# Optimization experiments

Hardware: AMD Instinct MI355X
Metric: run time of the kernel (lower is better)

## Reference

```python
import jax, jax.numpy as jnp
import numpy as np

D_MODEL = 1024
NUM_HEADS = 16
D_K = D_MODEL // NUM_HEADS
B, T = 2, 2048


def setup_inputs() -> dict:
    key = jax.random.key(0)
    ks = jax.random.split(key, 9)
    s = 1.0 / np.sqrt(D_MODEL)
    inp = {"x": jax.random.normal(ks[0], (B, T, D_MODEL), dtype=jnp.float32)}
    for i, name in enumerate(["q", "k", "v", "out"]):
        inp[f"W_{name}"] = jax.random.uniform(ks[1 + 2 * i], (D_MODEL, D_MODEL), jnp.float32, -s, s)
        inp[f"b_{name}"] = jax.random.uniform(ks[2 + 2 * i], (D_MODEL,), jnp.float32, -s, s)
    return inp


def reference(x, W_q, b_q, W_k, b_k, W_v, b_v, W_out, b_out):
    b, t, _ = x.shape
    # torch Linear: y = x @ W.T + b
    def proj(inp, W, bias):
        y = inp @ W.T + bias
        return y.reshape(b, -1, NUM_HEADS, D_K).transpose(0, 2, 1, 3)  # [B,H,T,d_k]

    Q = proj(x, W_q, b_q)
    K = proj(x, W_k, b_k)
    V = proj(x, W_v, b_v)
    scores = jnp.einsum("bhqd,bhkd->bhqk", Q, K) / jnp.sqrt(jnp.float32(D_K))
    attn = jax.nn.softmax(scores, axis=-1)
    ctx = jnp.einsum("bhqk,bhkd->bhqd", attn, V)
    ctx = ctx.transpose(0, 2, 1, 3).reshape(b, t, D_MODEL)
    return ctx @ W_out.T + b_out
```

## Files before the change

### kernel.cpp

```cpp
#include <hip/hip_runtime.h>
#include <hip/hip_bf16.h>

typedef __attribute__((ext_vector_type(8))) short short8;
typedef __attribute__((ext_vector_type(4))) short short4v;
typedef __attribute__((ext_vector_type(4))) float floatx4;

__device__ __forceinline__ unsigned short f2b(float f) {
  unsigned int v;
  __builtin_memcpy(&v, &f, 4);
  unsigned int r = (v + 0x7FFFu + ((v >> 16) & 1u)) >> 16;
  return (unsigned short)r;
}

__device__ __forceinline__ unsigned int f2b_pk(float a, float b) {
#if __has_builtin(__builtin_amdgcn_cvt_pk_bf16_f32)
  typedef __attribute__((ext_vector_type(2))) __bf16 bf16x2;
  bf16x2 r = __builtin_amdgcn_cvt_pk_bf16_f32(a, b);
  unsigned int u;
  __builtin_memcpy(&u, &r, 4);
  return u;
#else
  return ((unsigned int)f2b(b) << 16) | (unsigned int)f2b(a);
#endif
}

__device__ __forceinline__ float fast_exp2(float x) {
#if __has_builtin(__builtin_amdgcn_exp2f)
  return __builtin_amdgcn_exp2f(x);
#else
  return __builtin_exp2f(x);
#endif
}

__device__ __forceinline__ void async_copy16(const void* g, void* l) {
  __builtin_amdgcn_global_load_lds(
      (const __attribute__((address_space(1))) unsigned int*)g,
      (__attribute__((address_space(3))) unsigned int*)l, 16, 0, 0);
}

#define QSCALE 0.18033688011112042f

__global__ __launch_bounds__(256) void cvt_all_kernel(
    const float* __restrict__ x,
    const float* __restrict__ w0, const float* __restrict__ w1,
    const float* __restrict__ w2, const float* __restrict__ w3,
    unsigned short* __restrict__ xb,
    unsigned short* __restrict__ d0, unsigned short* __restrict__ d1,
    unsigned short* __restrict__ d2, unsigned short* __restrict__ d3)
{
  int gid = blockIdx.x * 256 + threadIdx.x;
  const float* src;
  unsigned short* dst;
  size_t off;
  if (gid < (1 << 20)) {
    src = x; dst = xb; off = gid;
  } else {
    int g = gid - (1 << 20);
    int w = g >> 18;
    off = g & 0x3FFFF;
    src = (w == 0) ? w0 : (w == 1) ? w1 : (w == 2) ? w2 : w3;
    dst = (w == 0) ? d0 : (w == 1) ? d1 : (w == 2) ? d2 : d3;
  }
  floatx4 v = *(const floatx4*)(src + off * 4);
  unsigned int lo = f2b_pk(v[0], v[1]), hi = f2b_pk(v[2], v[3]);
  unsigned long long r = ((unsigned long long)hi << 32) | lo;
  *(unsigned long long*)(dst + off * 4) = r;
}

__global__ __launch_bounds__(256) void gemm_qkv_kernel(
    const unsigned short* __restrict__ A,
    const unsigned short* __restrict__ W0, const unsigned short* __restrict__ W1,
    const unsigned short* __restrict__ W2,
    const float* __restrict__ bias0, const float* __restrict__ bias1,
    const float* __restrict__ bias2,
    unsigned short* __restrict__ Qo, unsigned short* __restrict__ Ko,
    unsigned short* __restrict__ VTo)
{
  const int z = blockIdx.z;
  const unsigned short* W  = (z == 0) ? W0 : (z == 1) ? W1 : W2;
  const float* bias        = (z == 0) ? bias0 : (z == 1) ? bias1 : bias2;

  __shared__ alignas(16) unsigned short sA[128 * 32];
  __shared__ alignas(16) unsigned short sB[128 * 32];

  const int tid  = threadIdx.x;
  const int lane = tid & 63;
  const int wave = tid >> 6;
  const int col  = lane & 15;
  const int quad = lane >> 4;
  const int wm   = (wave >> 1) * 64;
  const int wn   = (wave & 1) * 64;
  const int m0   = blockIdx.y * 128;
  const int n0   = blockIdx.x * 128;

  floatx4 acc[4][4];
#pragma unroll
  for (int i = 0; i < 4; ++i)
#pragma unroll
    for (int j = 0; j < 4; ++j) acc[i][j] = (floatx4){0.f, 0.f, 0.f, 0.f};

  for (int k0 = 0; k0 < 1024; k0 += 32) {
    __syncthreads();
#pragma unroll
    for (int i = 0; i < 2; ++i) {
      int c   = i * 256 + tid;
      int row = c >> 2;
      int ko  = (c & 3) * 8;
      async_copy16(A + (size_t)(m0 + row) * 1024 + k0 + ko, sA + c * 8);
      async_copy16(W + (size_t)(n0 + row) * 1024 + k0 + ko, sB + c * 8);
    }
    __syncthreads();
    short8 af[4], bf[4];
#pragma unroll
    for (int mi = 0; mi < 4; ++mi)
      af[mi] = *(const short8*)(sA + (wm + mi * 16 + col) * 32 + quad * 8);
#pragma unroll
    for (int ni = 0; ni < 4; ++ni)
      bf[ni] = *(const short8*)(sB + (wn + ni * 16 + col) * 32 + quad * 8);
#pragma unroll
    for (int mi = 0; mi < 4; ++mi)
#pragma unroll
      for (int ni = 0; ni < 4; ++ni)
        acc[mi][ni] = __builtin_amdgcn_mfma_f32_16x16x32_bf16(af[mi], bf[ni], acc[mi][ni], 0, 0, 0);
  }

#pragma unroll
  for (int ni = 0; ni < 4; ++ni) {
    int n = n0 + wn + ni * 16 + col;
    float bv = bias[n];
#pragma unroll
    for (int mi = 0; mi < 4; ++mi) {
      int mbase = m0 + wm + mi * 16 + quad * 4;
#pragma unroll
      for (int r = 0; r < 4; ++r) {
        int m = mbase + r;
        float val = acc[mi][ni][r] + bv;
        if (z == 0) {
          Qo[(size_t)m * 1024 + n] = f2b(val * QSCALE);
        } else if (z == 1) {
          Ko[(size_t)m * 1024 + n] = f2b(val);
        } else {
          int d = n & 63, h = n >> 6;
          int bb = m >> 11, t = m & 2047;
          VTo[(((size_t)bb * 16 + h) * 64 + d) * 2048 + t] = f2b(val);
        }
      }
    }
  }
}

__global__ __launch_bounds__(256) void gemm_out_kernel(
    const unsigned short* __restrict__ A, const unsigned short* __restrict__ W,
    const float* __restrict__ bias, float* __restrict__ DF)
{
  __shared__ alignas(16) unsigned short sA[128 * 32];
  __shared__ alignas(16) unsigned short sB[64 * 32];

  const int tid  = threadIdx.x;
  const int lane = tid & 63;
  const int wave = tid >> 6;
  const int col  = lane & 15;
  const int quad = lane >> 4;
  const int wm   = (wave >> 1) * 64;
  const int wn   = (wave & 1) * 32;
  const int m0   = blockIdx.y * 128;
  const int n0   = blockIdx.x * 64;

  floatx4 acc[4][2];
#pragma unroll
  for (int i = 0; i < 4; ++i)
#pragma unroll
    for (int j = 0; j < 2; ++j) acc[i][j] = (floatx4){0.f, 0.f, 0.f, 0.f};

  for (int k0 = 0; k0 < 1024; k0 += 32) {
    __syncthreads();
#pragma unroll
    for (int i = 0; i < 2; ++i) {
      int c   = i * 256 + tid;
      int row = c >> 2;
      int ko  = (c & 3) * 8;
      async_copy16(A + (size_t)(m0 + row) * 1024 + k0 + ko, sA + c * 8);
    }
    {
      int row = tid >> 2;
      int ko  = (tid & 3) * 8;
      async_copy16(W + (size_t)(n0 + row) * 1024 + k0 + ko, sB + tid * 8);
    }
    __syncthreads();
    short8 af[4], bf[2];
#pragma unroll
    for (int mi = 0; mi < 4; ++mi)
      af[mi] = *(const short8*)(sA + (wm + mi * 16 + col) * 32 + quad * 8);
#pragma unroll
    for (int ni = 0; ni < 2; ++ni)
      bf[ni] = *(const short8*)(sB + (wn + ni * 16 + col) * 32 + quad * 8);
#pragma unroll
    for (int mi = 0; mi < 4; ++mi)
#pragma unroll
      for (int ni = 0; ni < 2; ++ni)
        acc[mi][ni] = __builtin_amdgcn_mfma_f32_16x16x32_bf16(af[mi], bf[ni], acc[mi][ni], 0, 0, 0);
  }

#pragma unroll
  for (int ni = 0; ni < 2; ++ni) {
    int n = n0 + wn + ni * 16 + col;
    float bv = bias[n];
#pragma unroll
    for (int mi = 0; mi < 4; ++mi) {
      int mbase = m0 + wm + mi * 16 + quad * 4;
#pragma unroll
      for (int r = 0; r < 4; ++r)
        DF[(size_t)(mbase + r) * 1024 + n] = acc[mi][ni][r] + bv;
    }
  }
}

__global__ __launch_bounds__(256) void attention_kernel(
    const unsigned short* __restrict__ Q, const unsigned short* __restrict__ K,
    const unsigned short* __restrict__ VT, unsigned short* __restrict__ CTX)
{
  __shared__ alignas(16) unsigned short sKb[16384];
  __shared__ alignas(16) unsigned short sVb[8192];
  __shared__ alignas(16) unsigned short sPb[9216];
  __shared__ float sL[4][64];

  const int bh = blockIdx.x;
  const int b = bh >> 4, h = bh & 15;
  const int q0 = blockIdx.y * 64;
  const int tid  = threadIdx.x;
  const int lane = tid & 63;
  const int wave = tid >> 6;
  const int col  = lane & 15;
  const int quad = lane >> 4;
  const int l4   = lane >> 2;
  const int lo4  = (lane & 3) * 8;

  const unsigned short* Kg = K + (size_t)(b * 2048) * 1024 + h * 64;
  const unsigned short* Vg = VT + (size_t)bh * 64 * 2048;

#pragma unroll
  for (int s = 0; s < 2; ++s)
    async_copy16(Q + (size_t)(b * 2048 + q0 + wave * 16 + l4) * 1024 + h * 64 + s * 32 + lo4,
                 sPb + s * 2048 + wave * 512 + lane * 8);
  {
    unsigned short* kd = sKb + wave * 2048;
#pragma unroll
    for (int s = 0; s < 2; ++s)
#pragma unroll
      for (int j = 0; j < 2; ++j)
        async_copy16(Kg + (size_t)(wave * 32 + j * 16 + l4) * 1024 + s * 32 + lo4,
                     kd + s * 1024 + j * 512 + lane * 8);
    unsigned short* vd = sVb + wave * 2048;
#pragma unroll
    for (int i = 0; i < 4; ++i)
      async_copy16(Vg + (size_t)(i * 16 + l4) * 2048 + wave * 32 + lo4,
                   vd + i * 512 + lane * 8);
  }
  __builtin_amdgcn_s_waitcnt(0xF70);
  __syncthreads();

  short8 qf[4][2];
#pragma unroll
  for (int qc = 0; qc < 4; ++qc)
#pragma unroll
    for (int s = 0; s < 2; ++s)
      qf[qc][s] = *(const short8*)(sPb + s * 2048 + (qc * 16 + col) * 32 + quad * 8);
  __syncthreads();

  floatx4 Oacc[4][4];
#pragma unroll
  for (int mq = 0; mq < 4; ++mq)
#pragma unroll
    for (int nd = 0; nd < 4; ++nd) Oacc[mq][nd] = (floatx4){0.f, 0.f, 0.f, 0.f};
  float lacc[4] = {0.f, 0.f, 0.f, 0.f};
  unsigned short* myP = sPb + wave * 2304;
  unsigned short* vw  = sVb + wave * 2048;

  for (int t = 0; t < 16; ++t) {
    const int buf = t & 1;
    unsigned short* kw = sKb + buf * 8192 + wave * 2048;
    const int ktn = (t + 1) * 128;

    if (t < 15) {
      unsigned short* kd = sKb + (buf ^ 1) * 8192 + wave * 2048;
#pragma unroll
      for (int s = 0; s < 2; ++s)
#pragma unroll
        for (int j = 0; j < 2; ++j)
          async_copy16(Kg + (size_t)(ktn + wave * 32 + j * 16 + l4) * 1024 + s * 32 + lo4,
                       kd + s * 1024 + j * 512 + lane * 8);
      __builtin_amdgcn_s_waitcnt(0xF78);
    } else {
      __builtin_amdgcn_s_waitcnt(0xF74);
    }

    floatx4 ST[2][4];
#pragma unroll
    for (int kr = 0; kr < 2; ++kr)
#pragma unroll
      for (int qc = 0; qc < 4; ++qc) ST[kr][qc] = (floatx4){0.f, 0.f, 0.f, 0.f};
#pragma unroll
    for (int s = 0; s < 2; ++s) {
      short8 k0 = *(const short8*)(kw + s * 1024 + col * 32 + quad * 8);
      short8 k1 = *(const short8*)(kw + s * 1024 + (16 + col) * 32 + quad * 8);
#pragma unroll
      for (int qc = 0; qc < 4; ++qc) {
        ST[0][qc] = __builtin_amdgcn_mfma_f32_16x16x32_bf16(k0, qf[qc][s], ST[0][qc], 0, 0, 0);
        ST[1][qc] = __builtin_amdgcn_mfma_f32_16x16x32_bf16(k1, qf[qc][s], ST[1][qc], 0, 0, 0);
      }
    }

#pragma unroll
    for (int kr = 0; kr < 2; ++kr)
#pragma unroll
      for (int qc = 0; qc < 4; ++qc) {
        float p0 = fast_exp2(ST[kr][qc][0]);
        float p1 = fast_exp2(ST[kr][qc][1]);
        float p2 = fast_exp2(ST[kr][qc][2]);
        float p3 = fast_exp2(ST[kr][qc][3]);
        lacc[qc] += (p0 + p1) + (p2 + p3);
        unsigned long long pw =
            ((unsigned long long)f2b_pk(p2, p3) << 32) | f2b_pk(p0, p1);
        *(unsigned long long*)(myP + (qc * 16 + col) * 36 + kr * 16 + quad * 4) = pw;
      }

    short8 pf[4];
#pragma unroll
    for (int mq = 0; mq < 4; ++mq) {
      const unsigned short* pp = myP + (mq * 16 + col) * 36 + quad * 8;
      short4v plo = *(const short4v*)pp;
      short4v phi = *(const short4v*)(pp + 4);
      pf[mq] = (short8){plo[0], plo[1], plo[2], plo[3], phi[0], phi[1], phi[2], phi[3]};
    }

    if (t < 15) __builtin_amdgcn_s_waitcnt(0xF74);
    else        __builtin_amdgcn_s_waitcnt(0xF70);

    short8 vf[4];
#pragma unroll
    for (int nd = 0; nd < 4; ++nd)
      vf[nd] = *(const short8*)(vw + (nd * 16 + col) * 32 + quad * 8);
    __builtin_amdgcn_s_waitcnt(0xC07F);

    if (t < 15) {
#pragma unroll
      for (int i = 0; i < 4; ++i)
        async_copy16(Vg + (size_t)(i * 16 + l4) * 2048 + ktn + wave * 32 + lo4,
                     vw + i * 512 + lane * 8);
    }

#pragma unroll
    for (int nd = 0; nd < 4; ++nd)
#pragma unroll
      for (int mq = 0; mq < 4; ++mq)
        Oacc[mq][nd] = __builtin_amdgcn_mfma_f32_16x16x32_bf16(pf[mq], vf[nd], Oacc[mq][nd], 0, 0, 0);
  }

#pragma unroll
  for (int qc = 0; qc < 4; ++qc) {
    lacc[qc] += __shfl_xor(lacc[qc], 16, 64);
    lacc[qc] += __shfl_xor(lacc[qc], 32, 64);
  }
  if (quad == 0) {
#pragma unroll
    for (int qc = 0; qc < 4; ++qc) sL[wave][qc * 16 + col] = lacc[qc];
  }

  float* sO = (float*)sKb;
#pragma unroll 1
  for (int ww = 0; ww < 4; ++ww) {
    __syncthreads();
    if (wave == ww) {
#pragma unroll
      for (int mq = 0; mq < 4; ++mq)
#pragma unroll
        for (int nd = 0; nd < 4; ++nd)
#pragma unroll
          for (int r = 0; r < 4; ++r) {
            int idx = (mq * 16 + quad * 4 + r) * 64 + nd * 16 + col;
            if (ww == 0) sO[idx] = Oacc[mq][nd][r];
            else         sO[idx] += Oacc[mq][nd][r];
          }
    }
  }
  __syncthreads();

  {
    int q = tid >> 2, c = tid & 3;
    float l = sL[0][q] + sL[1][q] + sL[2][q] + sL[3][q];
    float inv = 1.f / l;
    const float* row = sO + q * 64 + c * 16;
    unsigned short* dst = CTX + (size_t)(b * 2048 + q0 + q) * 1024 + h * 64 + c * 16;
#pragma unroll
    for (int hf = 0; hf < 2; ++hf) {
      alignas(16) unsigned short ob[8];
#pragma unroll
      for (int j = 0; j < 8; ++j) ob[j] = f2b(row[hf * 8 + j] * inv);
      *(short8*)(dst + hf * 8) = *(const short8*)ob;
    }
  }
}

extern "C" void kernel_launch(void* const* d_in, const int* in_sizes, int n_in,
                              void* d_out, int out_size, void* d_ws, size_t ws_size,
                              hipStream_t stream) {
  const float* x   = (const float*)d_in[0];
  const float* W_q = (const float*)d_in[1];
  const float* b_q = (const float*)d_in[2];
  const float* W_k = (const float*)d_in[3];
  const float* b_k = (const float*)d_in[4];
  const float* W_v = (const float*)d_in[5];
  const float* b_v = (const float*)d_in[6];
  const float* W_o = (const float*)d_in[7];
  const float* b_o = (const float*)d_in[8];
  float* out = (float*)d_out;

  const size_t NX = (size_t)4096 * 1024;
  const size_t NW = (size_t)1024 * 1024;

  unsigned short* p   = (unsigned short*)d_ws;
  unsigned short* xb  = p;  p += NX;
  unsigned short* Wqb = p;  p += NW;
  unsigned short* Wkb = p;  p += NW;
  unsigned short* Wvb = p;  p += NW;
  unsigned short* Wob = p;  p += NW;
  unsigned short* Q   = p;  p += NX;
  unsigned short* Kb  = p;  p += NX;
  unsigned short* VT  = p;  p += NX;
  unsigned short* CTX = p;  p += NX;

  dim3 blk(256);
  cvt_all_kernel<<<dim3(8192), blk, 0, stream>>>(
      x, W_q, W_k, W_v, W_o, xb, Wqb, Wkb, Wvb, Wob);
  gemm_qkv_kernel<<<dim3(8, 32, 3), blk, 0, stream>>>(
      xb, Wqb, Wkb, Wvb, b_q, b_k, b_v, Q, Kb, VT);
  attention_kernel<<<dim3(32, 32), blk, 0, stream>>>(Q, Kb, VT, CTX);
  gemm_out_kernel<<<dim3(16, 32), blk, 0, stream>>>(CTX, Wob, b_o, out);
}
```

Measured before the change: 229.2 us.

## Load K/V fragments directly to registers and keep P in registers via transposed MFMA

The attention kernel drops the shared-memory staging of K and V tiles and the async copies. Each wave now loads its K and V MFMA fragments straight from global memory into double-buffered registers. The second GEMM is computed transposed (V^T times P), so the bf16 probabilities feed the MFMA from registers instead of round-tripping through LDS. Launch bounds request two blocks per SM. In exchange, global loads are less coalesced, register pressure is higher, and latency hiding now depends on the register prefetch.

```diff
diff --git a/kernel.cpp b/kernel.cpp
--- a/kernel.cpp
+++ b/kernel.cpp
@@ -215,13 +215,11 @@
   }
 }
 
-__global__ __launch_bounds__(256) void attention_kernel(
+__global__ __launch_bounds__(256, 2) void attention_kernel(
     const unsigned short* __restrict__ Q, const unsigned short* __restrict__ K,
     const unsigned short* __restrict__ VT, unsigned short* __restrict__ CTX)
 {
-  __shared__ alignas(16) unsigned short sKb[16384];
-  __shared__ alignas(16) unsigned short sVb[8192];
-  __shared__ alignas(16) unsigned short sPb[9216];
+  __shared__ float sO[64 * 64];
   __shared__ float sL[4][64];
 
   const int bh = blockIdx.x;
@@ -232,129 +230,97 @@
   const int wave = tid >> 6;
   const int col  = lane & 15;
   const int quad = lane >> 4;
-  const int l4   = lane >> 2;
-  const int lo4  = (lane & 3) * 8;
-
-  const unsigned short* Kg = K + (size_t)(b * 2048) * 1024 + h * 64;
-  const unsigned short* Vg = VT + (size_t)bh * 64 * 2048;
-
-#pragma unroll
-  for (int s = 0; s < 2; ++s)
-    async_copy16(Q + (size_t)(b * 2048 + q0 + wave * 16 + l4) * 1024 + h * 64 + s * 32 + lo4,
-                 sPb + s * 2048 + wave * 512 + lane * 8);
-  {
-    unsigned short* kd = sKb + wave * 2048;
+
+  const unsigned short* Kg  = K + ((size_t)b * 2048) * 1024 + h * 64;
+  const unsigned short* VTg = VT + (size_t)bh * 64 * 2048;
+
+  short8 qf[4][2];
+#pragma unroll
+  for (int qc = 0; qc < 4; ++qc)
 #pragma unroll
     for (int s = 0; s < 2; ++s)
-#pragma unroll
-      for (int j = 0; j < 2; ++j)
-        async_copy16(Kg + (size_t)(wave * 32 + j * 16 + l4) * 1024 + s * 32 + lo4,
-                     kd + s * 1024 + j * 512 + lane * 8);
-    unsigned short* vd = sVb + wave * 2048;
-#pragma unroll
-    for (int i = 0; i < 4; ++i)
-      async_copy16(Vg + (size_t)(i * 16 + l4) * 2048 + wave * 32 + lo4,
-                   vd + i * 512 + lane * 8);
-  }
-  __builtin_amdgcn_s_waitcnt(0xF70);
-  __syncthreads();
-
-  short8 qf[4][2];
-#pragma unroll
-  for (int qc = 0; qc < 4; ++qc)
-#pragma unroll
-    for (int s = 0; s < 2; ++s)
-      qf[qc][s] = *(const short8*)(sPb + s * 2048 + (qc * 16 + col) * 32 + quad * 8);
-  __syncthreads();
+      qf[qc][s] = *(const short8*)(Q + (size_t)(b * 2048 + q0 + qc * 16 + col) * 1024
+                                    + h * 64 + s * 32 + quad * 8);
 
   floatx4 Oacc[4][4];
 #pragma unroll
-  for (int mq = 0; mq < 4; ++mq)
-#pragma unroll
-    for (int nd = 0; nd < 4; ++nd) Oacc[mq][nd] = (floatx4){0.f, 0.f, 0.f, 0.f};
+  for (int nd = 0; nd < 4; ++nd)
+#pragma unroll
+    for (int qc = 0; qc < 4; ++qc) Oacc[nd][qc] = (floatx4){0.f, 0.f, 0.f, 0.f};
   float lacc[4] = {0.f, 0.f, 0.f, 0.f};
-  unsigned short* myP = sPb + wave * 2304;
-  unsigned short* vw  = sVb + wave * 2048;
-
+
+  short8  kfb[2][2][2];
+  short4v vfb[2][4][2];
+
+  const int ksl = wave * 32;
+
+#define LOAD_K(buf, kt)                                                        \
+  {                                                                            \
+    _Pragma("unroll") for (int kr = 0; kr < 2; ++kr)                           \
+      _Pragma("unroll") for (int s = 0; s < 2; ++s)                            \
+        kfb[buf][kr][s] = *(const short8*)(                                    \
+            Kg + (size_t)((kt) + ksl + kr * 16 + col) * 1024 + s * 32 + quad * 8); \
+  }
+#define LOAD_V(buf, kt)                                                        \
+  {                                                                            \
+    _Pragma("unroll") for (int nd = 0; nd < 4; ++nd)                           \
+      _Pragma("unroll") for (int hf = 0; hf < 2; ++hf)                         \
+        vfb[buf][nd][hf] = *(const short4v*)(                                  \
+            VTg + (size_t)(nd * 16 + col) * 2048 + (kt) + ksl + hf * 16 + quad * 4); \
+  }
+
+  LOAD_K(0, 0)
+  LOAD_V(0, 0)
+
+#pragma unroll 2
   for (int t = 0; t < 16; ++t) {
-    const int buf = t & 1;
-    unsigned short* kw = sKb + buf * 8192 + wave * 2048;
-    const int ktn = (t + 1) * 128;
-
+    const int cur = t & 1, nxt = cur ^ 1;
     if (t < 15) {
-      unsigned short* kd = sKb + (buf ^ 1) * 8192 + wave * 2048;
-#pragma unroll
-      for (int s = 0; s < 2; ++s)
-#pragma unroll
-        for (int j = 0; j < 2; ++j)
-          async_copy16(Kg + (size_t)(ktn + wave * 32 + j * 16 + l4) * 1024 + s * 32 + lo4,
-                       kd + s * 1024 + j * 512 + lane * 8);
-      __builtin_amdgcn_s_waitcnt(0xF78);
-    } else {
-      __builtin_amdgcn_s_waitcnt(0xF74);
+      LOAD_K(nxt, (t + 1) * 128)
+      LOAD_V(nxt, (t + 1) * 128)
     }
 
     floatx4 ST[2][4];
 #pragma unroll
     for (int kr = 0; kr < 2; ++kr)
 #pragma unroll
-      for (int qc = 0; qc < 4; ++qc) ST[kr][qc] = (floatx4){0.f, 0.f, 0.f, 0.f};
-#pragma unroll
-    for (int s = 0; s < 2; ++s) {
-      short8 k0 = *(const short8*)(kw + s * 1024 + col * 32 + quad * 8);
-      short8 k1 = *(const short8*)(kw + s * 1024 + (16 + col) * 32 + quad * 8);
-#pragma unroll
       for (int qc = 0; qc < 4; ++qc) {
-        ST[0][qc] = __builtin_amdgcn_mfma_f32_16x16x32_bf16(k0, qf[qc][s], ST[0][qc], 0, 0, 0);
-        ST[1][qc] = __builtin_amdgcn_mfma_f32_16x16x32_bf16(k1, qf[qc][s], ST[1][qc], 0, 0, 0);
+        ST[kr][qc] = (floatx4){0.f, 0.f, 0.f, 0.f};
+        ST[kr][qc] = __builtin_amdgcn_mfma_f32_16x16x32_bf16(
+            kfb[cur][kr][0], qf[qc][0], ST[kr][qc], 0, 0, 0);
+        ST[kr][qc] = __builtin_amdgcn_mfma_f32_16x16x32_bf16(
+            kfb[cur][kr][1], qf[qc][1], ST[kr][qc], 0, 0, 0);
       }
-    }
-
-#pragma unroll
-    for (int kr = 0; kr < 2; ++kr)
-#pragma unroll
-      for (int qc = 0; qc < 4; ++qc) {
-        float p0 = fast_exp2(ST[kr][qc][0]);
-        float p1 = fast_exp2(ST[kr][qc][1]);
-        float p2 = fast_exp2(ST[kr][qc][2]);
-        float p3 = fast_exp2(ST[kr][qc][3]);
-        lacc[qc] += (p0 + p1) + (p2 + p3);
-        unsigned long long pw =
-            ((unsigned long long)f2b_pk(p2, p3) << 32) | f2b_pk(p0, p1);
-        *(unsigned long long*)(myP + (qc * 16 + col) * 36 + kr * 16 + quad * 4) = pw;
-      }
 
     short8 pf[4];
 #pragma unroll
-    for (int mq = 0; mq < 4; ++mq) {
-      const unsigned short* pp = myP + (mq * 16 + col) * 36 + quad * 8;
-      short4v plo = *(const short4v*)pp;
-      short4v phi = *(const short4v*)(pp + 4);
-      pf[mq] = (short8){plo[0], plo[1], plo[2], plo[3], phi[0], phi[1], phi[2], phi[3]};
-    }
-
-    if (t < 15) __builtin_amdgcn_s_waitcnt(0xF74);
-    else        __builtin_amdgcn_s_waitcnt(0xF70);
-
-    short8 vf[4];
-#pragma unroll
-    for (int nd = 0; nd < 4; ++nd)
-      vf[nd] = *(const short8*)(vw + (nd * 16 + col) * 32 + quad * 8);
-    __builtin_amdgcn_s_waitcnt(0xC07F);
-
-    if (t < 15) {
-#pragma unroll
-      for (int i = 0; i < 4; ++i)
-        async_copy16(Vg + (size_t)(i * 16 + l4) * 2048 + ktn + wave * 32 + lo4,
-                     vw + i * 512 + lane * 8);
-    }
-
-#pragma unroll
-    for (int nd = 0; nd < 4; ++nd)
-#pragma unroll
-      for (int mq = 0; mq < 4; ++mq)
-        Oacc[mq][nd] = __builtin_amdgcn_mfma_f32_16x16x32_bf16(pf[mq], vf[nd], Oacc[mq][nd], 0, 0, 0);
-  }
+    for (int qc = 0; qc < 4; ++qc) {
+      float p00 = fast_exp2(ST[0][qc][0]);
+      float p01 = fast_exp2(ST[0][qc][1]);
+      float p02 = fast_exp2(ST[0][qc][2]);
+      float p03 = fast_exp2(ST[0][qc][3]);
+      float p10 = fast_exp2(ST[1][qc][0]);
+      float p11 = fast_exp2(ST[1][qc][1]);
+      float p12 = fast_exp2(ST[1][qc][2]);
+      float p13 = fast_exp2(ST[1][qc][3]);
+      lacc[qc] += ((p00 + p01) + (p02 + p03)) + ((p10 + p11) + (p12 + p13));
+      alignas(16) unsigned int d4[4] = {
+          f2b_pk(p00, p01), f2b_pk(p02, p03), f2b_pk(p10, p11), f2b_pk(p12, p13)};
+      __builtin_memcpy(&pf[qc], d4, 16);
+    }
+
+#pragma unroll
+    for (int nd = 0; nd < 4; ++nd) {
+      short8 vf = __builtin_shufflevector(vfb[cur][nd][0], vfb[cur][nd][1],
+                                          0, 1, 2, 3, 4, 5, 6, 7);
+#pragma unroll
+      for (int qc = 0; qc < 4; ++qc)
+        Oacc[nd][qc] = __builtin_amdgcn_mfma_f32_16x16x32_bf16(
+            vf, pf[qc], Oacc[nd][qc], 0, 0, 0);
+    }
+  }
+#undef LOAD_K
+#undef LOAD_V
 
 #pragma unroll
   for (int qc = 0; qc < 4; ++qc) {
@@ -366,20 +332,19 @@
     for (int qc = 0; qc < 4; ++qc) sL[wave][qc * 16 + col] = lacc[qc];
   }
 
-  float* sO = (float*)sKb;
 #pragma unroll 1
   for (int ww = 0; ww < 4; ++ww) {
     __syncthreads();
     if (wave == ww) {
 #pragma unroll
-      for (int mq = 0; mq < 4; ++mq)
-#pragma unroll
-        for (int nd = 0; nd < 4; ++nd)
+      for (int nd = 0; nd < 4; ++nd)
+#pragma unroll
+        for (int qc = 0; qc < 4; ++qc)
 #pragma unroll
           for (int r = 0; r < 4; ++r) {
-            int idx = (mq * 16 + quad * 4 + r) * 64 + nd * 16 + col;
-            if (ww == 0) sO[idx] = Oacc[mq][nd][r];
-            else         sO[idx] += Oacc[mq][nd][r];
+            int idx = (qc * 16 + col) * 64 + nd * 16 + quad * 4 + r;
+            if (ww == 0) sO[idx] = Oacc[nd][qc][r];
+            else         sO[idx] += Oacc[nd][qc][r];
           }
     }
   }
```

Result: slower. 268.3 us (+17.1%).
